# Kernel tuning notes

Measured on AMD Instinct MI355X. Metric: run time of the kernel, lower is better.

Reference implementation:

```python
import jax, jax.numpy as jnp
import numpy as np


def lut_quantize(v, lut):
    """Nearest-neighbor LUT quantization with straight-through estimator.
    lut is sorted ascending; uses searchsorted (no [N, L] blowup)."""
    L = lut.shape[0]
    idx = jnp.clip(jnp.searchsorted(lut, v), 1, L - 1)
    left = jnp.take(lut, idx - 1)
    right = jnp.take(lut, idx)
    q = jnp.where(v - left <= right - v, left, right)
    return v + jax.lax.stop_gradient(q - v)


def mem_conv(x, w, b, lut):
    # memConv2d: weights/bias snapped to LUT levels, then standard 3x3 SAME conv (NCHW/OIHW)
    wq = lut_quantize(w, lut)
    bq = lut_quantize(b, lut)
    y = jax.lax.conv_general_dilated(x, wq, window_strides=(1, 1),
                                     padding=((1, 1), (1, 1)),
                                     dimension_numbers=('NCHW', 'OIHW', 'NCHW'))
    return y + bq[None, :, None, None]


def mem_linear(x, w, b, lut):
    # memLinear: torch-style weight (out, in)
    return x @ lut_quantize(w, lut).T + lut_quantize(b, lut)


def mem_relu(x, lut):
    # memReLu: ReLU followed by LUT quantization of the activation
    return lut_quantize(jnp.maximum(x, 0.0), lut)


def max_pool_2x2(x):
    return jax.lax.reduce_window(x, -jnp.inf, jax.lax.max,
                                 (1, 1, 2, 2), (1, 1, 2, 2), 'VALID')


def _forward(x, lut, w1, b1, w2, b2, w3, b3, w4, b4, w5, b5, w6, b6,
             fw1, fb1, fw2, fb2, fw3, fb3):
    x = mem_relu(mem_conv(x, w1, b1, lut), lut)
    x = mem_relu(mem_conv(x, w2, b2, lut), lut)
    x = max_pool_2x2(x)                      # [B,32,16,16]
    x = mem_relu(mem_conv(x, w3, b3, lut), lut)
    x = mem_relu(mem_conv(x, w4, b4, lut), lut)
    x = max_pool_2x2(x)                      # [B,64,8,8]
    x = mem_relu(mem_conv(x, w5, b5, lut), lut)
    x = mem_relu(mem_conv(x, w6, b6, lut), lut)
    x = max_pool_2x2(x)                      # [B,128,4,4]
    x = x.reshape(-1, 128 * 4 * 4)
    x = mem_relu(mem_linear(x, fw1, fb1, lut), lut)
    x = mem_relu(mem_linear(x, fw2, fb2, lut), lut)
    x = mem_linear(x, fw3, fb3, lut)
    return jax.nn.softmax(x, axis=1)


def setup_inputs() -> dict:
    key = jax.random.key(0)
    ks = jax.random.split(key, 20)
    B = 512
    lut = jnp.linspace(-4.0, 4.0, 129).astype(jnp.float32)

    def conv_w(k, co, ci):
        scale = np.sqrt(2.0 / (ci * 9)).astype(np.float32)
        return jax.random.normal(k, (co, ci, 3, 3), jnp.float32) * scale

    def lin_w(k, co, ci):
        scale = np.sqrt(2.0 / ci).astype(np.float32)
        return jax.random.normal(k, (co, ci), jnp.float32) * scale

    return {
        'x': jax.random.normal(ks[0], (B, 3, 32, 32), jnp.float32),
        'lut': lut,
        'w1': conv_w(ks[1], 32, 3),   'b1': jnp.zeros((32,), jnp.float32),
        'w2': conv_w(ks[2], 32, 32),  'b2': jnp.zeros((32,), jnp.float32),
        'w3': conv_w(ks[3], 64, 32),  'b3': jnp.zeros((64,), jnp.float32),
        'w4': conv_w(ks[4], 64, 64),  'b4': jnp.zeros((64,), jnp.float32),
        'w5': conv_w(ks[5], 128, 64), 'b5': jnp.zeros((128,), jnp.float32),
        'w6': conv_w(ks[6], 128, 128),'b6': jnp.zeros((128,), jnp.float32),
        'fw1': lin_w(ks[7], 512, 2048), 'fb1': jnp.zeros((512,), jnp.float32),
        'fw2': lin_w(ks[8], 128, 512),  'fb2': jnp.zeros((128,), jnp.float32),
        'fw3': lin_w(ks[9], 10, 128),   'fb3': jnp.zeros((10,), jnp.float32),
    }


def reference(x, lut, w1, b1, w2, b2, w3, b3, w4, b4, w5, b5, w6, b6,
              fw1, fb1, fw2, fb2, fw3, fb3):
    return _forward(x, lut, w1, b1, w2, b2, w3, b3, w4, b4, w5, b5, w6, b6,
                    fw1, fb1, fw2, fb2, fw3, fb3)
```

## Files before the change

### kernel.cpp

```cpp
#include <hip/hip_runtime.h>
#include <cstddef>


#define B_SZ 512
typedef unsigned int u32;
typedef __attribute__((ext_vector_type(4))) int i32x4;

__device__ __forceinline__ float lutq(float v) {
    float k = ceilf(v * 16.0f - 0.5f);
    k = fminf(64.0f, fmaxf(-64.0f, k));
    return k * 0.0625f;
}
__device__ __forceinline__ int kq(float x) {
    float kf = ceilf(x * 16.0f - 0.5f);
    kf = fminf(64.0f, fmaxf(-64.0f, kf));
    return (int)kf;
}
__device__ __forceinline__ u32 bmax4u(u32 a, u32 b) {
    u32 r = 0;
    #pragma unroll
    for (int j = 0; j < 4; ++j) {
        u32 x = (a >> (8 * j)) & 255u, y = (b >> (8 * j)) & 255u;
        r |= (x > y ? x : y) << (8 * j);
    }
    return r;
}
__device__ __forceinline__ int requant(int s, int kb16) {
    int vv = s + kb16;
    vv = vv > 0 ? vv : 0;
    int kk = (vv + 7) >> 4;
    return kk > 64 ? 64 : kk;
}

__device__ __forceinline__ void prep_conv_frag(const float* __restrict__ w, char* __restrict__ q,
                                               int i, int CI) {
    int NSTEP = (9 * CI + 63) / 64;
    int e = i & 15, t = i >> 4;
    int ln = t & 63, t2 = t >> 6;
    int s = t2 % NSTEP, co_tile = t2 / NSTEP;
    int k = s * 64 + ((ln >> 4) << 4) + e;
    int tap = k / CI, ci = k % CI;
    int co = co_tile * 16 + (ln & 15);
    int val = 0;
    if (tap < 9) val = kq(w[(co * CI + ci) * 9 + tap]);
    q[i] = (char)val;
}
__device__ __forceinline__ void prep_fc_frag(const float* __restrict__ w, char* __restrict__ q,
                                             int i, int K) {
    int S = K >> 6;
    int e = i & 15, t = i >> 4;
    int ln = t & 63, t2 = t >> 6;
    int s = t2 % S, n_tile = t2 / S;
    int n = n_tile * 16 + (ln & 15);
    int k = s * 64 + ((ln >> 4) << 4) + e;
    q[i] = (char)kq(w[(size_t)n * K + k]);
}

__global__ __launch_bounds__(256) void prep_conv1(
    const float* __restrict__ w2, const float* __restrict__ w3, const float* __restrict__ w4,
    const float* __restrict__ w5, const float* __restrict__ w6,
    const float* __restrict__ fw1, const float* __restrict__ fw2,
    char* q2, char* q3, char* q4, char* q5, char* q6, char* qf1, char* qf2,
    const float* __restrict__ x, const float* __restrict__ w1,
    const float* __restrict__ b1, char* __restrict__ out)
{
    const int tid = threadIdx.x;
    const int bid = blockIdx.x;
    if (bid < 5480) {
        int i = bid * 256 + tid;
        if (i < 10240)                  { prep_conv_frag(w2, q2, i, 32);  }
        else if ((i -= 10240) < 20480)  { prep_conv_frag(w3, q3, i, 32);  }
        else if ((i -= 20480) < 36864)  { prep_conv_frag(w4, q4, i, 64);  }
        else if ((i -= 36864) < 73728)  { prep_conv_frag(w5, q5, i, 64);  }
        else if ((i -= 73728) < 147456) { prep_conv_frag(w6, q6, i, 128); }
        else if ((i -= 147456) < 1048576){ prep_fc_frag(fw1, qf1, i, 2048); }
        else if ((i -= 1048576) < 65536) { prep_fc_frag(fw2, qf2, i, 512);  }
        return;
    }
    __shared__ float s_w[3][9][32];
    __shared__ float s_b[32];
    __shared__ float s_in[3][10][34];
    const int bx  = bid - 5480;
    const int b   = bx >> 2;
    const int r0  = (bx & 3) * 8;
    for (int i = tid; i < 864; i += 256) {
        int o = i % 32, k = (i / 32) % 9, c = i / 288;
        s_w[c][k][o] = lutq(w1[(o * 3 + c) * 9 + k]);
    }
    if (tid < 32) s_b[tid] = lutq(b1[tid]);
    for (int i = tid; i < 3 * 10 * 34; i += 256) {
        int xx = i % 34, yy = (i / 34) % 10, c = i / 340;
        int gy = r0 + yy - 1, gx = xx - 1;
        float v = 0.f;
        if ((unsigned)gy < 32u && (unsigned)gx < 32u)
            v = x[(((size_t)b * 3 + c) * 32 + gy) * 32 + gx];
        s_in[c][yy][xx] = v;
    }
    __syncthreads();
    const int y = tid >> 5, xx = tid & 31;
    float acc[32];
    #pragma unroll
    for (int o = 0; o < 32; ++o) acc[o] = 0.f;
    #pragma unroll
    for (int c = 0; c < 3; ++c) {
        #pragma unroll
        for (int k = 0; k < 9; ++k) {
            float iv = s_in[c][y + k / 3][xx + k % 3];
            #pragma unroll
            for (int o = 0; o < 32; ++o) acc[o] = fmaf(iv, s_w[c][k][o], acc[o]);
        }
    }
    u32 u[8];
    #pragma unroll
    for (int j = 0; j < 8; ++j) {
        u32 p = 0;
        #pragma unroll
        for (int q = 0; q < 4; ++q) {
            float v = fmaxf(acc[4 * j + q] + s_b[4 * j + q], 0.f);
            int kk = (int)ceilf(v * 16.0f - 0.5f);
            kk = kk > 64 ? 64 : kk;
            p |= ((u32)kk & 255u) << (8 * q);
        }
        u[j] = p;
    }
    const int p = (b << 10) + ((r0 + y) << 5) + xx;
    u32* o4 = (u32*)(out + (size_t)p * 32);
    #pragma unroll
    for (int j = 0; j < 8; ++j) o4[j] = u[j];
}

template<int HW, int CI, int CO, int RS, int NIMG, int NT, int POOL = 0>
__global__ __launch_bounds__(256) void conv_mfma(
    const char* __restrict__ in, const char* __restrict__ wq,
    const float* __restrict__ bias, char* __restrict__ out)
{
    constexpr int PH  = HW + 2;
    constexpr int PIX = NIMG * (RS + 2) * PH;
    constexpr int M   = NIMG * RS * HW;
    constexpr int MT  = M / 16;
    constexpr int MW  = MT / 4;
    constexpr int NSTEP = (9 * CI + 63) / 64;
    constexpr int SL  = HW / RS;
    constexpr int NC16 = CI / 16;
    constexpr int NTC = NT * 16;

    __shared__ __align__(128) char s_in[PIX * CI];

    const int tid = threadIdx.x;
    const int g   = blockIdx.x;
    const int b0  = (g / SL) * NIMG;
    const int r0  = (g % SL) * RS;
    const int co0 = blockIdx.y * NTC;

    constexpr int TOTC = PIX * NC16;
    for (int i = tid; i < TOTC; i += 256) {
        int c16 = i % NC16;
        int pp  = i / NC16;
        int xx  = pp % PH;
        int rr  = pp / PH;
        int yy  = rr % (RS + 2);
        int img = rr / (RS + 2);
        int gy = r0 + yy - 1, gx = xx - 1;
        uint4 v = {0u, 0u, 0u, 0u};
        if ((unsigned)gy < (unsigned)HW && (unsigned)gx < (unsigned)HW)
            v = *(const uint4*)(in + ((((size_t)(b0 + img) * HW + gy) * HW + gx) * CI + c16 * 16));
        int off = (pp * CI + c16 * 16) ^ ((pp & 7) << 4);
        *(uint4*)(s_in + off) = v;
    }
    __syncthreads();

    const int wv = tid >> 6, ln = tid & 63;
    const int l15 = ln & 15, lq = ln >> 4;

    int ppad[MW];
    #pragma unroll
    for (int mw = 0; mw < MW; ++mw) {
        int p = (wv * MW + mw) * 16 + l15;
        int img = p / (RS * HW);
        int rem = p % (RS * HW);
        int ly = rem / HW, lx = rem % HW;
        ppad[mw] = (img * (RS + 2) + ly + 1) * PH + lx + 1;
    }

    i32x4 acc[MW][NT] = {};
    const char* wtile = wq + ((size_t)blockIdx.y * NT) * NSTEP * 1024 + (ln << 4);
    auto dp = [](int t) { return (t / 3 - 1) * PH + (t % 3 - 1); };

    #pragma unroll
    for (int s = 0; s < NSTEP; ++s) {
        i32x4 bf[NT];
        #pragma unroll
        for (int nt = 0; nt < NT; ++nt)
            bf[nt] = *(const i32x4*)(wtile + ((nt * NSTEP + s) << 10));
        int dd, ci0;
        if constexpr (CI == 32) {
            int d0 = dp(2 * s);
            int d1 = (2 * s + 1 < 9) ? dp(2 * s + 1) : 0;
            dd  = (lq & 2) ? d1 : d0;
            ci0 = (lq & 1) << 4;
        } else if constexpr (CI == 64) {
            dd  = dp(s);
            ci0 = lq << 4;
        } else {
            dd  = dp(s >> 1);
            ci0 = ((s & 1) << 6) + (lq << 4);
        }
        #pragma unroll
        for (int mw = 0; mw < MW; ++mw) {
            int pix = ppad[mw] + dd;
            int off = (pix * CI + ci0) ^ ((pix & 7) << 4);
            i32x4 af = *(const i32x4*)(s_in + off);
            #pragma unroll
            for (int nt = 0; nt < NT; ++nt)
                acc[mw][nt] = __builtin_amdgcn_mfma_i32_16x16x64_i8(af, bf[nt], acc[mw][nt], 0, 0, 0);
        }
    }

    if constexpr (POOL == 0) {
        #pragma unroll
        for (int nt = 0; nt < NT; ++nt) {
            int kb16 = 16 * kq(bias[co0 + nt * 16 + l15]);
            #pragma unroll
            for (int mw = 0; mw < MW; ++mw)
                #pragma unroll
                for (int r = 0; r < 4; ++r) {
                    int p = (wv * MW + mw) * 16 + lq * 4 + r;
                    int img = p / (RS * HW), rem = p % (RS * HW);
                    int ly = rem / HW, lx = rem % HW;
                    out[(((size_t)(b0 + img) * HW + r0 + ly) * HW + lx) * CO + co0 + nt * 16 + l15] =
                        (char)requant(acc[mw][nt][r], kb16);
                }
        }
    } else {
        __syncthreads();
        char* s_out = s_in;
        #pragma unroll
        for (int nt = 0; nt < NT; ++nt) {
            int kb16 = 16 * kq(bias[co0 + nt * 16 + l15]);
            #pragma unroll
            for (int mw = 0; mw < MW; ++mw)
                #pragma unroll
                for (int r = 0; r < 4; ++r) {
                    int p = (wv * MW + mw) * 16 + lq * 4 + r;
                    s_out[p * NTC + nt * 16 + l15] = (char)requant(acc[mw][nt][r], kb16);
                }
        }
        __syncthreads();
        constexpr int PR = RS / 2, PC = HW / 2, HOW = HW / 2;
        constexpr int OCT = NIMG * PR * PC * (NTC / 16);
        for (int idx = tid; idx < OCT; idx += 256) {
            int c16 = idx % (NTC / 16);
            int pp  = idx / (NTC / 16);
            int xo = pp % PC, yo = (pp / PC) % PR, img = pp / (PC * PR);
            int pb = (img * RS + 2 * yo) * HW + 2 * xo;
            uint4 v0 = *(const uint4*)(s_out + (pb)          * NTC + c16 * 16);
            uint4 v1 = *(const uint4*)(s_out + (pb + 1)      * NTC + c16 * 16);
            uint4 v2 = *(const uint4*)(s_out + (pb + HW)     * NTC + c16 * 16);
            uint4 v3 = *(const uint4*)(s_out + (pb + HW + 1) * NTC + c16 * 16);
            uint4 r;
            r.x = bmax4u(bmax4u(v0.x, v1.x), bmax4u(v2.x, v3.x));
            r.y = bmax4u(bmax4u(v0.y, v1.y), bmax4u(v2.y, v3.y));
            r.z = bmax4u(bmax4u(v0.z, v1.z), bmax4u(v2.z, v3.z));
            r.w = bmax4u(bmax4u(v0.w, v1.w), bmax4u(v2.w, v3.w));
            *(uint4*)(out + ((((size_t)(b0 + img) * HOW + (r0 >> 1) + yo) * HOW + xo) * CO
                             + co0 + c16 * 16)) = r;
        }
    }
}

__global__ __launch_bounds__(256) void conv34(
    const char* __restrict__ in,
    const char* __restrict__ q3, const float* __restrict__ b3,
    const char* __restrict__ q4, const float* __restrict__ b4,
    char* __restrict__ out)
{
    __shared__ __align__(128) char s_in[18 * 18 * 32];
    __shared__ __align__(128) char mid[18 * 18 * 64];
    const int tid = threadIdx.x;
    const int b   = blockIdx.x;
    const int wv = tid >> 6, ln = tid & 63, l15 = ln & 15, lq = ln >> 4;

    for (int i = tid; i < 648; i += 256) {
        int c16 = i & 1;
        int pp  = i >> 1;
        int xx = pp % 18, yy = pp / 18;
        int gy = yy - 1, gx = xx - 1;
        uint4 v = {0u, 0u, 0u, 0u};
        if ((unsigned)gy < 16u && (unsigned)gx < 16u)
            v = *(const uint4*)(in + (((size_t)b * 16 + gy) * 16 + gx) * 32 + c16 * 16);
        int off = (pp * 32 + c16 * 16) ^ ((pp & 7) << 4);
        *(uint4*)(s_in + off) = v;
    }
    for (int i = tid; i < 5184; i += 256) ((u32*)mid)[i] = 0u;
    __syncthreads();

    int ppad[4];
    #pragma unroll
    for (int mw = 0; mw < 4; ++mw) {
        int p = (wv * 4 + mw) * 16 + l15;
        ppad[mw] = ((p >> 4) + 1) * 18 + (p & 15) + 1;
    }
    auto dp18 = [](int t) { return (t / 3 - 1) * 18 + (t % 3 - 1); };

    i32x4 acc3[4][4] = {};
    #pragma unroll
    for (int s = 0; s < 5; ++s) {
        i32x4 bf[4];
        #pragma unroll
        for (int nt = 0; nt < 4; ++nt)
            bf[nt] = *(const i32x4*)(q3 + ((nt * 5 + s) << 10) + (ln << 4));
        int d0 = dp18(2 * s);
        int d1 = (2 * s + 1 < 9) ? dp18(2 * s + 1) : 0;
        int dd = (lq & 2) ? d1 : d0;
        int ci0 = (lq & 1) << 4;
        #pragma unroll
        for (int mw = 0; mw < 4; ++mw) {
            int pix = ppad[mw] + dd;
            int off = (pix * 32 + ci0) ^ ((pix & 7) << 4);
            i32x4 af = *(const i32x4*)(s_in + off);
            #pragma unroll
            for (int nt = 0; nt < 4; ++nt)
                acc3[mw][nt] = __builtin_amdgcn_mfma_i32_16x16x64_i8(af, bf[nt], acc3[mw][nt], 0, 0, 0);
        }
    }
    #pragma unroll
    for (int nt = 0; nt < 4; ++nt) {
        int kb16 = 16 * kq(b3[nt * 16 + l15]);
        #pragma unroll
        for (int mw = 0; mw < 4; ++mw)
            #pragma unroll
            for (int r = 0; r < 4; ++r) {
                int p = (wv * 4 + mw) * 16 + lq * 4 + r;
                int pix = ((p >> 4) + 1) * 18 + (p & 15) + 1;
                mid[(pix * 64 + nt * 16 + l15) ^ ((pix & 7) << 4)] =
                    (char)requant(acc3[mw][nt][r], kb16);
            }
    }
    __syncthreads();

    i32x4 acc4[4][4] = {};
    #pragma unroll
    for (int s = 0; s < 9; ++s) {
        i32x4 bf[4];
        #pragma unroll
        for (int nt = 0; nt < 4; ++nt)
            bf[nt] = *(const i32x4*)(q4 + ((nt * 9 + s) << 10) + (ln << 4));
        int dd = dp18(s);
        int ci0 = lq << 4;
        #pragma unroll
        for (int mw = 0; mw < 4; ++mw) {
            int pix = ppad[mw] + dd;
            int off = (pix * 64 + ci0) ^ ((pix & 7) << 4);
            i32x4 af = *(const i32x4*)(mid + off);
            #pragma unroll
            for (int nt = 0; nt < 4; ++nt)
                acc4[mw][nt] = __builtin_amdgcn_mfma_i32_16x16x64_i8(af, bf[nt], acc4[mw][nt], 0, 0, 0);
        }
    }
    __syncthreads();
    char* s_out = mid;
    #pragma unroll
    for (int nt = 0; nt < 4; ++nt) {
        int kb16 = 16 * kq(b4[nt * 16 + l15]);
        #pragma unroll
        for (int mw = 0; mw < 4; ++mw)
            #pragma unroll
            for (int r = 0; r < 4; ++r) {
                int p = (wv * 4 + mw) * 16 + lq * 4 + r;
                s_out[p * 64 + nt * 16 + l15] = (char)requant(acc4[mw][nt][r], kb16);
            }
    }
    __syncthreads();
    {
        int c16 = tid & 3;
        int pp  = tid >> 2;
        int xo = pp & 7, yo = pp >> 3;
        int pb = (2 * yo) * 16 + 2 * xo;
        uint4 v0 = *(const uint4*)(s_out + (pb)      * 64 + c16 * 16);
        uint4 v1 = *(const uint4*)(s_out + (pb + 1)  * 64 + c16 * 16);
        uint4 v2 = *(const uint4*)(s_out + (pb + 16) * 64 + c16 * 16);
        uint4 v3 = *(const uint4*)(s_out + (pb + 17) * 64 + c16 * 16);
        uint4 r;
        r.x = bmax4u(bmax4u(v0.x, v1.x), bmax4u(v2.x, v3.x));
        r.y = bmax4u(bmax4u(v0.y, v1.y), bmax4u(v2.y, v3.y));
        r.z = bmax4u(bmax4u(v0.z, v1.z), bmax4u(v2.z, v3.z));
        r.w = bmax4u(bmax4u(v0.w, v1.w), bmax4u(v2.w, v3.w));
        *(uint4*)(out + (((size_t)b * 8 + yo) * 8 + xo) * 64 + c16 * 16) = r;
    }
}

__global__ __launch_bounds__(256) void conv56(
    const char* __restrict__ in,
    const char* __restrict__ q5, const float* __restrict__ b5,
    const char* __restrict__ q6, const float* __restrict__ b6,
    char* __restrict__ fc1a)
{
    __shared__ __align__(128) char sA[8192];
    __shared__ __align__(128) char sB[12800];
    const int tid = threadIdx.x;
    const int b   = blockIdx.x;
    const int wv = tid >> 6, ln = tid & 63, l15 = ln & 15, lq = ln >> 4;

    for (int i = tid; i < 400; i += 256) {
        int c16 = i & 3;
        int pp  = i >> 2;
        int xx = pp % 10, yy = pp / 10;
        int gy = yy - 1, gx = xx - 1;
        uint4 v = {0u, 0u, 0u, 0u};
        if ((unsigned)gy < 8u && (unsigned)gx < 8u)
            v = *(const uint4*)(in + (((size_t)b * 8 + gy) * 8 + gx) * 64 + c16 * 16);
        int off = (pp * 64 + c16 * 16) ^ ((pp & 7) << 4);
        *(uint4*)(sA + off) = v;
    }
    for (int i = tid; i < 3200; i += 256) ((u32*)sB)[i] = 0u;
    __syncthreads();

    const int p0 = wv * 16 + l15;
    const int ppad = ((p0 >> 3) + 1) * 10 + (p0 & 7) + 1;
    auto dp10 = [](int t) { return (t / 3 - 1) * 10 + (t % 3 - 1); };

    i32x4 acc5[8] = {};
    #pragma unroll
    for (int s = 0; s < 9; ++s) {
        i32x4 bf[8];
        #pragma unroll
        for (int nt = 0; nt < 8; ++nt)
            bf[nt] = *(const i32x4*)(q5 + ((nt * 9 + s) << 10) + (ln << 4));
        int dd = dp10(s);
        int ci0 = lq << 4;
        int pix = ppad + dd;
        int off = (pix * 64 + ci0) ^ ((pix & 7) << 4);
        i32x4 af = *(const i32x4*)(sA + off);
        #pragma unroll
        for (int nt = 0; nt < 8; ++nt)
            acc5[nt] = __builtin_amdgcn_mfma_i32_16x16x64_i8(af, bf[nt], acc5[nt], 0, 0, 0);
    }
    #pragma unroll
    for (int nt = 0; nt < 8; ++nt) {
        int kb16 = 16 * kq(b5[nt * 16 + l15]);
        #pragma unroll
        for (int r = 0; r < 4; ++r) {
            int p = wv * 16 + lq * 4 + r;
            int pix = ((p >> 3) + 1) * 10 + (p & 7) + 1;
            sB[(pix * 128 + nt * 16 + l15) ^ ((pix & 7) << 4)] =
                (char)requant(acc5[nt][r], kb16);
        }
    }
    __syncthreads();

    i32x4 acc6[8] = {};
    #pragma unroll
    for (int s = 0; s < 18; ++s) {
        i32x4 bf[8];
        #pragma unroll
        for (int nt = 0; nt < 8; ++nt)
            bf[nt] = *(const i32x4*)(q6 + ((nt * 18 + s) << 10) + (ln << 4));
        int dd = dp10(s >> 1);
        int ci0 = ((s & 1) << 6) + (lq << 4);
        int pix = ppad + dd;
        int off = (pix * 128 + ci0) ^ ((pix & 7) << 4);
        i32x4 af = *(const i32x4*)(sB + off);
        #pragma unroll
        for (int nt = 0; nt < 8; ++nt)
            acc6[nt] = __builtin_amdgcn_mfma_i32_16x16x64_i8(af, bf[nt], acc6[nt], 0, 0, 0);
    }
    __syncthreads();
    char* s_out = sA;
    #pragma unroll
    for (int nt = 0; nt < 8; ++nt) {
        int kb16 = 16 * kq(b6[nt * 16 + l15]);
        #pragma unroll
        for (int r = 0; r < 4; ++r) {
            int p = wv * 16 + lq * 4 + r;
            s_out[p * 128 + nt * 16 + l15] = (char)requant(acc6[nt][r], kb16);
        }
    }
    __syncthreads();
    if (tid < 128) {
        int c16 = tid & 7;
        int pp  = tid >> 3;
        int xo = pp & 3, yo = pp >> 2;
        int pb = (2 * yo) * 8 + 2 * xo;
        uint4 v0 = *(const uint4*)(s_out + (pb)     * 128 + c16 * 16);
        uint4 v1 = *(const uint4*)(s_out + (pb + 1) * 128 + c16 * 16);
        uint4 v2 = *(const uint4*)(s_out + (pb + 8) * 128 + c16 * 16);
        uint4 v3 = *(const uint4*)(s_out + (pb + 9) * 128 + c16 * 16);
        uint4 r;
        r.x = bmax4u(bmax4u(v0.x, v1.x), bmax4u(v2.x, v3.x));
        r.y = bmax4u(bmax4u(v0.y, v1.y), bmax4u(v2.y, v3.y));
        r.z = bmax4u(bmax4u(v0.z, v1.z), bmax4u(v2.z, v3.z));
        r.w = bmax4u(bmax4u(v0.w, v1.w), bmax4u(v2.w, v3.w));
        const char* rv = (const char*)&r;
        int m = b;
        #pragma unroll
        for (int j = 0; j < 16; ++j) {
            int c = c16 * 16 + j;
            int k = c * 16 + yo * 4 + xo;
            int off = (((m >> 4) * 32 + (k >> 6)) << 10)
                    + ((((k >> 4) & 3) * 16 + (m & 15)) << 4) + (k & 15);
            fc1a[off] = rv[j];
        }
    }
}

template<int N, int K, int SK>
__global__ __launch_bounds__(256) void fc1_splitk(
    const char* __restrict__ xa, const char* __restrict__ wq, int* __restrict__ part)
{
    constexpr int KCH = K / SK;
    constexpr int KS = K / 64;
    const int tid = threadIdx.x, wv = tid >> 6, ln = tid & 63;
    const int l15 = ln & 15, lq = ln >> 4;
    const int m0 = blockIdx.x * 128, n0 = blockIdx.y * 128;
    const int kb = blockIdx.z * KCH;
    const int mq = (wv >> 1) * 4, nq = (wv & 1) * 4;
    i32x4 acc[4][4] = {};
    const char* xr[4];
    const char* wt[4];
    #pragma unroll
    for (int t = 0; t < 4; ++t) {
        xr[t] = xa + (size_t)((m0 >> 4) + mq + t) * KS * 1024 + (ln << 4);
        wt[t] = wq + (size_t)((n0 >> 4) + nq + t) * KS * 1024 + (ln << 4);
    }
    for (int k0 = 0; k0 < KCH; k0 += 64) {
        const int s = (kb + k0) >> 6;
        i32x4 a[4], b[4];
        #pragma unroll
        for (int t = 0; t < 4; ++t) {
            a[t] = *(const i32x4*)(xr[t] + (s << 10));
            b[t] = *(const i32x4*)(wt[t] + (s << 10));
        }
        #pragma unroll
        for (int i = 0; i < 4; ++i)
            #pragma unroll
            for (int j = 0; j < 4; ++j)
                acc[i][j] = __builtin_amdgcn_mfma_i32_16x16x64_i8(a[i], b[j], acc[i][j], 0, 0, 0);
    }
    int* pb = part + (size_t)blockIdx.z * (B_SZ * N);
    #pragma unroll
    for (int j = 0; j < 4; ++j) {
        int n = n0 + (nq + j) * 16 + l15;
        #pragma unroll
        for (int i = 0; i < 4; ++i)
            #pragma unroll
            for (int r = 0; r < 4; ++r) {
                int m = m0 + (mq + i) * 16 + lq * 4 + r;
                pb[(size_t)m * N + n] = acc[i][j][r];
            }
    }
}

template<int N, int SK>
__global__ __launch_bounds__(256) void fc_reduce(
    const int* __restrict__ part, const float* __restrict__ bias, char* __restrict__ out)
{
    int i = blockIdx.x * 256 + threadIdx.x;
    if (i >= B_SZ * N) return;
    int s = 0;
    #pragma unroll
    for (int k = 0; k < SK; ++k) s += part[(size_t)k * (B_SZ * N) + i];
    out[i] = (char)requant(s, 16 * kq(bias[i % N]));
}

__global__ __launch_bounds__(256) void fc_tail(
    const char* __restrict__ x, const char* __restrict__ qf2,
    const float* __restrict__ fb2, const float* __restrict__ fw3,
    const float* __restrict__ fb3, float* __restrict__ out)
{
    __shared__ __align__(16) char sx[16 * 512];
    __shared__ __align__(16) char sy[16 * 128];
    __shared__ __align__(16) char sw3[10 * 128];
    __shared__ float sb3[10];
    __shared__ int sp[16][16][10];

    const int tid = threadIdx.x;
    const int m0 = blockIdx.x * 16;

    for (int idx = tid; idx < 512; idx += 256) {
        int r = idx >> 5, c16 = idx & 31;
        uint4 v = *(const uint4*)(x + (size_t)(m0 + r) * 512 + c16 * 16);
        *(uint4*)(sx + ((r * 512 + c16 * 16) ^ ((r & 7) << 4))) = v;
    }
    for (int i = tid; i < 1280; i += 256) sw3[i] = (char)kq(fw3[i]);
    if (tid < 10) sb3[tid] = lutq(fb3[tid]);
    __syncthreads();

    const int wv = tid >> 6, ln = tid & 63, l15 = ln & 15, lq = ln >> 4;
    const int ntg = wv * 2;
    i32x4 acc[2] = {};
    #pragma unroll
    for (int s = 0; s < 8; ++s) {
        int row = l15;
        i32x4 a = *(const i32x4*)(sx + ((row * 512 + s * 64 + lq * 16) ^ ((row & 7) << 4)));
        #pragma unroll
        for (int nt = 0; nt < 2; ++nt) {
            i32x4 b = *(const i32x4*)(qf2 + (((ntg + nt) * 8 + s) << 10) + (ln << 4));
            acc[nt] = __builtin_amdgcn_mfma_i32_16x16x64_i8(a, b, acc[nt], 0, 0, 0);
        }
    }
    #pragma unroll
    for (int nt = 0; nt < 2; ++nt) {
        int n = (ntg + nt) * 16 + l15;
        int kb16 = 16 * kq(fb2[n]);
        #pragma unroll
        for (int r = 0; r < 4; ++r) {
            int row = lq * 4 + r;
            sy[(row * 128 + n) ^ ((row & 7) << 4)] = (char)requant(acc[nt][r], kb16);
        }
    }
    __syncthreads();

    {
        int r = tid >> 4, g = tid & 15;
        uint2 yv = *(const uint2*)(sy + ((r * 128 + g * 8) ^ ((r & 7) << 4)));
        const char* yb = (const char*)&yv;
        #pragma unroll
        for (int o = 0; o < 10; ++o) {
            uint2 wv2 = *(const uint2*)(sw3 + o * 128 + g * 8);
            const char* wb = (const char*)&wv2;
            int S = 0;
            #pragma unroll
            for (int e = 0; e < 8; ++e) S += (int)yb[e] * (int)wb[e];
            sp[r][g][o] = S;
        }
    }
    __syncthreads();

    if (tid < 16) {
        int r = tid;
        float d[10];
        #pragma unroll
        for (int o = 0; o < 10; ++o) {
            int S = 0;
            #pragma unroll
            for (int g = 0; g < 16; ++g) S += sp[r][g][o];
            d[o] = (float)S * 0.00390625f + sb3[o];
        }
        float m = d[0];
        #pragma unroll
        for (int o = 1; o < 10; ++o) m = fmaxf(m, d[o]);
        float e[10];
        float sum = 0.f;
        #pragma unroll
        for (int o = 0; o < 10; ++o) { e[o] = expf(d[o] - m); sum += e[o]; }
        #pragma unroll
        for (int o = 0; o < 10; ++o) out[(size_t)(m0 + r) * 10 + o] = e[o] / sum;
    }
}

extern "C" void kernel_launch(void* const* d_in, const int* in_sizes, int n_in,
                              void* d_out, int out_size, void* d_ws, size_t ws_size,
                              hipStream_t stream)
{
    const float* x   = (const float*)d_in[0];
    const float* w1  = (const float*)d_in[2];
    const float* b1  = (const float*)d_in[3];
    const float* w2  = (const float*)d_in[4];
    const float* b2  = (const float*)d_in[5];
    const float* w3  = (const float*)d_in[6];
    const float* b3  = (const float*)d_in[7];
    const float* w4  = (const float*)d_in[8];
    const float* b4  = (const float*)d_in[9];
    const float* w5  = (const float*)d_in[10];
    const float* b5  = (const float*)d_in[11];
    const float* w6  = (const float*)d_in[12];
    const float* b6  = (const float*)d_in[13];
    const float* fw1 = (const float*)d_in[14];
    const float* fb1 = (const float*)d_in[15];
    const float* fw2 = (const float*)d_in[16];
    const float* fb2 = (const float*)d_in[17];
    const float* fw3 = (const float*)d_in[18];
    const float* fb3 = (const float*)d_in[19];
    float* out = (float*)d_out;

    char* bufA = (char*)d_ws;
    char* bufB = bufA + (16u << 20);
    char* q2  = bufB + (16u << 20);
    char* q3  = q2 + 10240;
    char* q4  = q3 + 20480;
    char* q5  = q4 + 36864;
    char* q6  = q5 + 73728;
    char* qf1 = q6 + 147456;
    char* qf2 = qf1 + 1048576;
    int*  part = (int*)(qf2 + 65536);
    char* fc1out = (char*)part + (16u << 20);
    char* fc1a   = fc1out + 262144;

    dim3 blk(256);

    prep_conv1<<<dim3(7528), blk, 0, stream>>>(
        w2, w3, w4, w5, w6, fw1, fw2, q2, q3, q4, q5, q6, qf1, qf2,
        x, w1, b1, bufA);
    conv_mfma<32, 32, 32, 8, 1, 2, 1><<<dim3(2048, 1), blk, 0, stream>>>(bufA, q2, b2, bufB);
    conv34<<<dim3(512), blk, 0, stream>>>(bufB, q3, b3, q4, b4, bufA);
    conv56<<<dim3(512), blk, 0, stream>>>(bufA, q5, b5, q6, b6, fc1a);
    fc1_splitk<512, 2048, 16><<<dim3(4, 4, 16), blk, 0, stream>>>(fc1a, qf1, part);
    fc_reduce<512, 16><<<dim3(1024), blk, 0, stream>>>(part, fb1, fc1out);
    fc_tail<<<dim3(32), blk, 0, stream>>>(fc1out, qf2, fb2, fw3, fb3, out);
}
```

Measured before the change: 97.43 us.

## Fuse all six conv layers into one per-image megakernel and fold FC1 reduce into tail

Replaces the separate conv1, conv2, conv34 and conv56 kernels with a single kernel that keeps each image's activations in shared memory through all conv and pooling stages. This removes the global-memory round trips of intermediate int8 activations and several kernel launches. The split-K reduction for FC1 is also folded into the tail kernel. The trade-off is only 512 blocks with about 64KB of shared memory each, which limits occupancy. The FC1 reduction is now done by just 32 blocks that read 16 partial sums per element.

```diff
diff --git a/kernel.cpp b/kernel.cpp
--- a/kernel.cpp
+++ b/kernel.cpp
@@ -56,441 +56,341 @@
     q[i] = (char)kq(w[(size_t)n * K + k]);
 }
 
-__global__ __launch_bounds__(256) void prep_conv1(
+__global__ __launch_bounds__(256) void prep_weights(
     const float* __restrict__ w2, const float* __restrict__ w3, const float* __restrict__ w4,
     const float* __restrict__ w5, const float* __restrict__ w6,
     const float* __restrict__ fw1, const float* __restrict__ fw2,
-    char* q2, char* q3, char* q4, char* q5, char* q6, char* qf1, char* qf2,
-    const float* __restrict__ x, const float* __restrict__ w1,
-    const float* __restrict__ b1, char* __restrict__ out)
+    char* q2, char* q3, char* q4, char* q5, char* q6, char* qf1, char* qf2)
 {
+    int i = blockIdx.x * 256 + threadIdx.x;
+    if (i < 10240)                  { prep_conv_frag(w2, q2, i, 32);  }
+    else if ((i -= 10240) < 20480)  { prep_conv_frag(w3, q3, i, 32);  }
+    else if ((i -= 20480) < 36864)  { prep_conv_frag(w4, q4, i, 64);  }
+    else if ((i -= 36864) < 73728)  { prep_conv_frag(w5, q5, i, 64);  }
+    else if ((i -= 73728) < 147456) { prep_conv_frag(w6, q6, i, 128); }
+    else if ((i -= 147456) < 1048576){ prep_fc_frag(fw1, qf1, i, 2048); }
+    else if ((i -= 1048576) < 65536) { prep_fc_frag(fw2, qf2, i, 512);  }
+}
+
+__global__ __launch_bounds__(256, 2) void megaconv(
+    const float* __restrict__ x, const float* __restrict__ w1, const float* __restrict__ b1,
+    const char* __restrict__ q2, const float* __restrict__ b2,
+    const char* __restrict__ q3, const float* __restrict__ b3,
+    const char* __restrict__ q4, const float* __restrict__ b4,
+    const char* __restrict__ q5, const float* __restrict__ b5,
+    const char* __restrict__ q6, const float* __restrict__ b6,
+    char* __restrict__ fc1a)
+{
+    __shared__ __align__(128) char smem[64816];
+    float* X  = (float*)smem;
+    float* SW = (float*)(smem + 13872);
+    float* SB = (float*)(smem + 17328);
+    char*  C1 = smem + 17456;
+    char*  C2 = smem;
+    char*  C3 = smem + 54448;
+    char*  C4 = smem;
+    char*  C5 = smem + 20736;
+    char*  C6 = smem + 54448;
+    char*  C7 = smem;
+    char*  C8 = smem + 12800;
+
     const int tid = threadIdx.x;
-    const int bid = blockIdx.x;
-    if (bid < 5480) {
-        int i = bid * 256 + tid;
-        if (i < 10240)                  { prep_conv_frag(w2, q2, i, 32);  }
-        else if ((i -= 10240) < 20480)  { prep_conv_frag(w3, q3, i, 32);  }
-        else if ((i -= 20480) < 36864)  { prep_conv_frag(w4, q4, i, 64);  }
-        else if ((i -= 36864) < 73728)  { prep_conv_frag(w5, q5, i, 64);  }
-        else if ((i -= 73728) < 147456) { prep_conv_frag(w6, q6, i, 128); }
-        else if ((i -= 147456) < 1048576){ prep_fc_frag(fw1, qf1, i, 2048); }
-        else if ((i -= 1048576) < 65536) { prep_fc_frag(fw2, qf2, i, 512);  }
-        return;
-    }
-    __shared__ float s_w[3][9][32];
-    __shared__ float s_b[32];
-    __shared__ float s_in[3][10][34];
-    const int bx  = bid - 5480;
-    const int b   = bx >> 2;
-    const int r0  = (bx & 3) * 8;
-    for (int i = tid; i < 864; i += 256) {
-        int o = i % 32, k = (i / 32) % 9, c = i / 288;
-        s_w[c][k][o] = lutq(w1[(o * 3 + c) * 9 + k]);
-    }
-    if (tid < 32) s_b[tid] = lutq(b1[tid]);
-    for (int i = tid; i < 3 * 10 * 34; i += 256) {
-        int xx = i % 34, yy = (i / 34) % 10, c = i / 340;
-        int gy = r0 + yy - 1, gx = xx - 1;
+    const int b   = blockIdx.x;
+    const int wv = tid >> 6, ln = tid & 63, l15 = ln & 15, lq = ln >> 4;
+
+    auto dp34 = [](int t) { return (t / 3 - 1) * 34 + (t % 3 - 1); };
+    auto dp18 = [](int t) { return (t / 3 - 1) * 18 + (t % 3 - 1); };
+    auto dp10 = [](int t) { return (t / 3 - 1) * 10 + (t % 3 - 1); };
+
+    for (int i = tid; i < 3468; i += 256) {
+        int xx = i % 34, t = i / 34, yy = t % 34, c = t / 34;
+        int gy = yy - 1, gx = xx - 1;
         float v = 0.f;
         if ((unsigned)gy < 32u && (unsigned)gx < 32u)
             v = x[(((size_t)b * 3 + c) * 32 + gy) * 32 + gx];
-        s_in[c][yy][xx] = v;
-    }
-    __syncthreads();
-    const int y = tid >> 5, xx = tid & 31;
-    float acc[32];
-    #pragma unroll
-    for (int o = 0; o < 32; ++o) acc[o] = 0.f;
-    #pragma unroll
-    for (int c = 0; c < 3; ++c) {
-        #pragma unroll
-        for (int k = 0; k < 9; ++k) {
-            float iv = s_in[c][y + k / 3][xx + k % 3];
-            #pragma unroll
-            for (int o = 0; o < 32; ++o) acc[o] = fmaf(iv, s_w[c][k][o], acc[o]);
-        }
-    }
-    u32 u[8];
-    #pragma unroll
-    for (int j = 0; j < 8; ++j) {
-        u32 p = 0;
-        #pragma unroll
-        for (int q = 0; q < 4; ++q) {
-            float v = fmaxf(acc[4 * j + q] + s_b[4 * j + q], 0.f);
-            int kk = (int)ceilf(v * 16.0f - 0.5f);
-            kk = kk > 64 ? 64 : kk;
-            p |= ((u32)kk & 255u) << (8 * q);
-        }
-        u[j] = p;
-    }
-    const int p = (b << 10) + ((r0 + y) << 5) + xx;
-    u32* o4 = (u32*)(out + (size_t)p * 32);
-    #pragma unroll
-    for (int j = 0; j < 8; ++j) o4[j] = u[j];
-}
-
-template<int HW, int CI, int CO, int RS, int NIMG, int NT, int POOL = 0>
-__global__ __launch_bounds__(256) void conv_mfma(
-    const char* __restrict__ in, const char* __restrict__ wq,
-    const float* __restrict__ bias, char* __restrict__ out)
-{
-    constexpr int PH  = HW + 2;
-    constexpr int PIX = NIMG * (RS + 2) * PH;
-    constexpr int M   = NIMG * RS * HW;
-    constexpr int MT  = M / 16;
-    constexpr int MW  = MT / 4;
-    constexpr int NSTEP = (9 * CI + 63) / 64;
-    constexpr int SL  = HW / RS;
-    constexpr int NC16 = CI / 16;
-    constexpr int NTC = NT * 16;
-
-    __shared__ __align__(128) char s_in[PIX * CI];
-
-    const int tid = threadIdx.x;
-    const int g   = blockIdx.x;
-    const int b0  = (g / SL) * NIMG;
-    const int r0  = (g % SL) * RS;
-    const int co0 = blockIdx.y * NTC;
-
-    constexpr int TOTC = PIX * NC16;
-    for (int i = tid; i < TOTC; i += 256) {
-        int c16 = i % NC16;
-        int pp  = i / NC16;
-        int xx  = pp % PH;
-        int rr  = pp / PH;
-        int yy  = rr % (RS + 2);
-        int img = rr / (RS + 2);
-        int gy = r0 + yy - 1, gx = xx - 1;
-        uint4 v = {0u, 0u, 0u, 0u};
-        if ((unsigned)gy < (unsigned)HW && (unsigned)gx < (unsigned)HW)
-            v = *(const uint4*)(in + ((((size_t)(b0 + img) * HW + gy) * HW + gx) * CI + c16 * 16));
-        int off = (pp * CI + c16 * 16) ^ ((pp & 7) << 4);
-        *(uint4*)(s_in + off) = v;
-    }
-    __syncthreads();
-
-    const int wv = tid >> 6, ln = tid & 63;
-    const int l15 = ln & 15, lq = ln >> 4;
-
-    int ppad[MW];
-    #pragma unroll
-    for (int mw = 0; mw < MW; ++mw) {
-        int p = (wv * MW + mw) * 16 + l15;
-        int img = p / (RS * HW);
-        int rem = p % (RS * HW);
-        int ly = rem / HW, lx = rem % HW;
-        ppad[mw] = (img * (RS + 2) + ly + 1) * PH + lx + 1;
-    }
-
-    i32x4 acc[MW][NT] = {};
-    const char* wtile = wq + ((size_t)blockIdx.y * NT) * NSTEP * 1024 + (ln << 4);
-    auto dp = [](int t) { return (t / 3 - 1) * PH + (t % 3 - 1); };
-
-    #pragma unroll
-    for (int s = 0; s < NSTEP; ++s) {
-        i32x4 bf[NT];
-        #pragma unroll
-        for (int nt = 0; nt < NT; ++nt)
-            bf[nt] = *(const i32x4*)(wtile + ((nt * NSTEP + s) << 10));
-        int dd, ci0;
-        if constexpr (CI == 32) {
-            int d0 = dp(2 * s);
-            int d1 = (2 * s + 1 < 9) ? dp(2 * s + 1) : 0;
-            dd  = (lq & 2) ? d1 : d0;
-            ci0 = (lq & 1) << 4;
-        } else if constexpr (CI == 64) {
-            dd  = dp(s);
-            ci0 = lq << 4;
-        } else {
-            dd  = dp(s >> 1);
-            ci0 = ((s & 1) << 6) + (lq << 4);
-        }
-        #pragma unroll
-        for (int mw = 0; mw < MW; ++mw) {
-            int pix = ppad[mw] + dd;
-            int off = (pix * CI + ci0) ^ ((pix & 7) << 4);
-            i32x4 af = *(const i32x4*)(s_in + off);
-            #pragma unroll
-            for (int nt = 0; nt < NT; ++nt)
-                acc[mw][nt] = __builtin_amdgcn_mfma_i32_16x16x64_i8(af, bf[nt], acc[mw][nt], 0, 0, 0);
-        }
-    }
-
-    if constexpr (POOL == 0) {
-        #pragma unroll
-        for (int nt = 0; nt < NT; ++nt) {
-            int kb16 = 16 * kq(bias[co0 + nt * 16 + l15]);
-            #pragma unroll
-            for (int mw = 0; mw < MW; ++mw)
+        X[i] = v;
+    }
+    for (int i = tid; i < 864; i += 256) {
+        int o = i % 32, k = (i / 32) % 9, c = i / 288;
+        SW[(c * 9 + k) * 32 + o] = lutq(w1[(o * 3 + c) * 9 + k]);
+    }
+    if (tid < 32) SB[tid] = lutq(b1[tid]);
+    for (int i = tid; i < 9248; i += 256) ((u32*)C1)[i] = 0u;
+    for (int i = tid; i < 2592; i += 256) ((u32*)C3)[i] = 0u;
+    __syncthreads();
+
+    for (int qq = 0; qq < 4; ++qq) {
+        int p = qq * 256 + tid;
+        int y = p >> 5, xc = p & 31;
+        float acc[32];
+        #pragma unroll
+        for (int o = 0; o < 32; ++o) acc[o] = 0.f;
+        #pragma unroll
+        for (int c = 0; c < 3; ++c)
+            #pragma unroll
+            for (int k = 0; k < 9; ++k) {
+                float iv = X[(c * 34 + y + k / 3) * 34 + xc + k % 3];
+                #pragma unroll
+                for (int o = 0; o < 32; ++o) acc[o] = fmaf(iv, SW[(c * 9 + k) * 32 + o], acc[o]);
+            }
+        int pix = (y + 1) * 34 + xc + 1;
+        #pragma unroll
+        for (int j = 0; j < 2; ++j) {
+            uint4 pk;
+            u32* pw = (u32*)&pk;
+            #pragma unroll
+            for (int h = 0; h < 4; ++h) {
+                u32 w = 0;
+                #pragma unroll
+                for (int e = 0; e < 4; ++e) {
+                    float v = fmaxf(acc[j * 16 + h * 4 + e] + SB[j * 16 + h * 4 + e], 0.f);
+                    int kk = (int)ceilf(v * 16.0f - 0.5f);
+                    kk = kk > 64 ? 64 : kk;
+                    w |= ((u32)kk & 255u) << (8 * e);
+                }
+                pw[h] = w;
+            }
+            *(uint4*)(C1 + ((pix * 32 + j * 16) ^ ((pix & 7) << 4))) = pk;
+        }
+    }
+    __syncthreads();
+
+    for (int r0 = 0; r0 < 32; r0 += 8) {
+        int ppad2[4];
+        #pragma unroll
+        for (int mw = 0; mw < 4; ++mw) {
+            int p = (wv * 4 + mw) * 16 + l15;
+            ppad2[mw] = (r0 + (p >> 5) + 1) * 34 + (p & 31) + 1;
+        }
+        i32x4 acc[4][2] = {};
+        #pragma unroll
+        for (int s = 0; s < 5; ++s) {
+            i32x4 bf[2];
+            #pragma unroll
+            for (int nt = 0; nt < 2; ++nt)
+                bf[nt] = *(const i32x4*)(q2 + (((nt * 5 + s) << 10) + (ln << 4)));
+            int d0 = dp34(2 * s);
+            int d1 = (2 * s + 1 < 9) ? dp34(2 * s + 1) : 0;
+            int dd = (lq & 2) ? d1 : d0;
+            int ci0 = (lq & 1) << 4;
+            #pragma unroll
+            for (int mw = 0; mw < 4; ++mw) {
+                int pix = ppad2[mw] + dd;
+                i32x4 af = *(const i32x4*)(C1 + ((pix * 32 + ci0) ^ ((pix & 7) << 4)));
+                #pragma unroll
+                for (int nt = 0; nt < 2; ++nt)
+                    acc[mw][nt] = __builtin_amdgcn_mfma_i32_16x16x64_i8(af, bf[nt], acc[mw][nt], 0, 0, 0);
+            }
+        }
+        #pragma unroll
+        for (int nt = 0; nt < 2; ++nt) {
+            int kb16 = 16 * kq(b2[nt * 16 + l15]);
+            #pragma unroll
+            for (int mw = 0; mw < 4; ++mw)
                 #pragma unroll
                 for (int r = 0; r < 4; ++r) {
-                    int p = (wv * MW + mw) * 16 + lq * 4 + r;
-                    int img = p / (RS * HW), rem = p % (RS * HW);
-                    int ly = rem / HW, lx = rem % HW;
-                    out[(((size_t)(b0 + img) * HW + r0 + ly) * HW + lx) * CO + co0 + nt * 16 + l15] =
-                        (char)requant(acc[mw][nt][r], kb16);
+                    int p = (wv * 4 + mw) * 16 + lq * 4 + r;
+                    C2[p * 32 + nt * 16 + l15] = (char)requant(acc[mw][nt][r], kb16);
                 }
         }
-    } else {
         __syncthreads();
-        char* s_out = s_in;
-        #pragma unroll
-        for (int nt = 0; nt < NT; ++nt) {
-            int kb16 = 16 * kq(bias[co0 + nt * 16 + l15]);
-            #pragma unroll
-            for (int mw = 0; mw < MW; ++mw)
-                #pragma unroll
-                for (int r = 0; r < 4; ++r) {
-                    int p = (wv * MW + mw) * 16 + lq * 4 + r;
-                    s_out[p * NTC + nt * 16 + l15] = (char)requant(acc[mw][nt][r], kb16);
-                }
+        if (tid < 128) {
+            int c16 = tid & 1;
+            int pp  = tid >> 1;
+            int xo = pp & 15, yo = pp >> 4;
+            int pb = (2 * yo) * 32 + 2 * xo;
+            uint4 v0 = *(const uint4*)(C2 + (pb)      * 32 + c16 * 16);
+            uint4 v1 = *(const uint4*)(C2 + (pb + 1)  * 32 + c16 * 16);
+            uint4 v2 = *(const uint4*)(C2 + (pb + 32) * 32 + c16 * 16);
+            uint4 v3 = *(const uint4*)(C2 + (pb + 33) * 32 + c16 * 16);
+            uint4 rr;
+            rr.x = bmax4u(bmax4u(v0.x, v1.x), bmax4u(v2.x, v3.x));
+            rr.y = bmax4u(bmax4u(v0.y, v1.y), bmax4u(v2.y, v3.y));
+            rr.z = bmax4u(bmax4u(v0.z, v1.z), bmax4u(v2.z, v3.z));
+            rr.w = bmax4u(bmax4u(v0.w, v1.w), bmax4u(v2.w, v3.w));
+            int py = (r0 >> 1) + yo;
+            int c3pix = (py + 1) * 18 + xo + 1;
+            *(uint4*)(C3 + ((c3pix * 32 + c16 * 16) ^ ((c3pix & 7) << 4))) = rr;
         }
         __syncthreads();
-        constexpr int PR = RS / 2, PC = HW / 2, HOW = HW / 2;
-        constexpr int OCT = NIMG * PR * PC * (NTC / 16);
-        for (int idx = tid; idx < OCT; idx += 256) {
-            int c16 = idx % (NTC / 16);
-            int pp  = idx / (NTC / 16);
-            int xo = pp % PC, yo = (pp / PC) % PR, img = pp / (PC * PR);
-            int pb = (img * RS + 2 * yo) * HW + 2 * xo;
-            uint4 v0 = *(const uint4*)(s_out + (pb)          * NTC + c16 * 16);
-            uint4 v1 = *(const uint4*)(s_out + (pb + 1)      * NTC + c16 * 16);
-            uint4 v2 = *(const uint4*)(s_out + (pb + HW)     * NTC + c16 * 16);
-            uint4 v3 = *(const uint4*)(s_out + (pb + HW + 1) * NTC + c16 * 16);
-            uint4 r;
-            r.x = bmax4u(bmax4u(v0.x, v1.x), bmax4u(v2.x, v3.x));
-            r.y = bmax4u(bmax4u(v0.y, v1.y), bmax4u(v2.y, v3.y));
-            r.z = bmax4u(bmax4u(v0.z, v1.z), bmax4u(v2.z, v3.z));
-            r.w = bmax4u(bmax4u(v0.w, v1.w), bmax4u(v2.w, v3.w));
-            *(uint4*)(out + ((((size_t)(b0 + img) * HOW + (r0 >> 1) + yo) * HOW + xo) * CO
-                             + co0 + c16 * 16)) = r;
-        }
-    }
-}
-
-__global__ __launch_bounds__(256) void conv34(
-    const char* __restrict__ in,
-    const char* __restrict__ q3, const float* __restrict__ b3,
-    const char* __restrict__ q4, const float* __restrict__ b4,
-    char* __restrict__ out)
-{
-    __shared__ __align__(128) char s_in[18 * 18 * 32];
-    __shared__ __align__(128) char mid[18 * 18 * 64];
-    const int tid = threadIdx.x;
-    const int b   = blockIdx.x;
-    const int wv = tid >> 6, ln = tid & 63, l15 = ln & 15, lq = ln >> 4;
-
-    for (int i = tid; i < 648; i += 256) {
-        int c16 = i & 1;
-        int pp  = i >> 1;
-        int xx = pp % 18, yy = pp / 18;
-        int gy = yy - 1, gx = xx - 1;
-        uint4 v = {0u, 0u, 0u, 0u};
-        if ((unsigned)gy < 16u && (unsigned)gx < 16u)
-            v = *(const uint4*)(in + (((size_t)b * 16 + gy) * 16 + gx) * 32 + c16 * 16);
-        int off = (pp * 32 + c16 * 16) ^ ((pp & 7) << 4);
-        *(uint4*)(s_in + off) = v;
-    }
-    for (int i = tid; i < 5184; i += 256) ((u32*)mid)[i] = 0u;
-    __syncthreads();
-
-    int ppad[4];
+    }
+
+    for (int i = tid; i < 5184; i += 256) ((u32*)C4)[i] = 0u;
+    __syncthreads();
+
+    int ppad16[4];
     #pragma unroll
     for (int mw = 0; mw < 4; ++mw) {
         int p = (wv * 4 + mw) * 16 + l15;
-        ppad[mw] = ((p >> 4) + 1) * 18 + (p & 15) + 1;
-    }
-    auto dp18 = [](int t) { return (t / 3 - 1) * 18 + (t % 3 - 1); };
-
-    i32x4 acc3[4][4] = {};
-    #pragma unroll
-    for (int s = 0; s < 5; ++s) {
-        i32x4 bf[4];
-        #pragma unroll
-        for (int nt = 0; nt < 4; ++nt)
-            bf[nt] = *(const i32x4*)(q3 + ((nt * 5 + s) << 10) + (ln << 4));
-        int d0 = dp18(2 * s);
-        int d1 = (2 * s + 1 < 9) ? dp18(2 * s + 1) : 0;
-        int dd = (lq & 2) ? d1 : d0;
-        int ci0 = (lq & 1) << 4;
-        #pragma unroll
-        for (int mw = 0; mw < 4; ++mw) {
-            int pix = ppad[mw] + dd;
-            int off = (pix * 32 + ci0) ^ ((pix & 7) << 4);
-            i32x4 af = *(const i32x4*)(s_in + off);
+        ppad16[mw] = ((p >> 4) + 1) * 18 + (p & 15) + 1;
+    }
+
+    {
+        i32x4 acc3[4][4] = {};
+        #pragma unroll
+        for (int s = 0; s < 5; ++s) {
+            i32x4 bf[4];
             #pragma unroll
             for (int nt = 0; nt < 4; ++nt)
-                acc3[mw][nt] = __builtin_amdgcn_mfma_i32_16x16x64_i8(af, bf[nt], acc3[mw][nt], 0, 0, 0);
-        }
-    }
-    #pragma unroll
-    for (int nt = 0; nt < 4; ++nt) {
-        int kb16 = 16 * kq(b3[nt * 16 + l15]);
-        #pragma unroll
-        for (int mw = 0; mw < 4; ++mw)
-            #pragma unroll
-            for (int r = 0; r < 4; ++r) {
-                int p = (wv * 4 + mw) * 16 + lq * 4 + r;
-                int pix = ((p >> 4) + 1) * 18 + (p & 15) + 1;
-                mid[(pix * 64 + nt * 16 + l15) ^ ((pix & 7) << 4)] =
-                    (char)requant(acc3[mw][nt][r], kb16);
-            }
-    }
-    __syncthreads();
-
-    i32x4 acc4[4][4] = {};
-    #pragma unroll
-    for (int s = 0; s < 9; ++s) {
-        i32x4 bf[4];
-        #pragma unroll
-        for (int nt = 0; nt < 4; ++nt)
-            bf[nt] = *(const i32x4*)(q4 + ((nt * 9 + s) << 10) + (ln << 4));
-        int dd = dp18(s);
-        int ci0 = lq << 4;
-        #pragma unroll
-        for (int mw = 0; mw < 4; ++mw) {
-            int pix = ppad[mw] + dd;
-            int off = (pix * 64 + ci0) ^ ((pix & 7) << 4);
-            i32x4 af = *(const i32x4*)(mid + off);
+                bf[nt] = *(const i32x4*)(q3 + (((nt * 5 + s) << 10) + (ln << 4)));
+            int d0 = dp18(2 * s);
+            int d1 = (2 * s + 1 < 9) ? dp18(2 * s + 1) : 0;
+            int dd = (lq & 2) ? d1 : d0;
+            int ci0 = (lq & 1) << 4;
+            #pragma unroll
+            for (int mw = 0; mw < 4; ++mw) {
+                int pix = ppad16[mw] + dd;
+                i32x4 af = *(const i32x4*)(C3 + ((pix * 32 + ci0) ^ ((pix & 7) << 4)));
+                #pragma unroll
+                for (int nt = 0; nt < 4; ++nt)
+                    acc3[mw][nt] = __builtin_amdgcn_mfma_i32_16x16x64_i8(af, bf[nt], acc3[mw][nt], 0, 0, 0);
+            }
+        }
+        #pragma unroll
+        for (int nt = 0; nt < 4; ++nt) {
+            int kb16 = 16 * kq(b3[nt * 16 + l15]);
+            #pragma unroll
+            for (int mw = 0; mw < 4; ++mw)
+                #pragma unroll
+                for (int r = 0; r < 4; ++r) {
+                    int p = (wv * 4 + mw) * 16 + lq * 4 + r;
+                    int pix = ((p >> 4) + 1) * 18 + (p & 15) + 1;
+                    C4[(pix * 64 + nt * 16 + l15) ^ ((pix & 7) << 4)] =
+                        (char)requant(acc3[mw][nt][r], kb16);
+                }
+        }
+    }
+    __syncthreads();
+
+    {
+        i32x4 acc4[4][4] = {};
+        #pragma unroll
+        for (int s = 0; s < 9; ++s) {
+            i32x4 bf[4];
             #pragma unroll
             for (int nt = 0; nt < 4; ++nt)
-                acc4[mw][nt] = __builtin_amdgcn_mfma_i32_16x16x64_i8(af, bf[nt], acc4[mw][nt], 0, 0, 0);
-        }
-    }
-    __syncthreads();
-    char* s_out = mid;
-    #pragma unroll
-    for (int nt = 0; nt < 4; ++nt) {
-        int kb16 = 16 * kq(b4[nt * 16 + l15]);
-        #pragma unroll
-        for (int mw = 0; mw < 4; ++mw)
-            #pragma unroll
-            for (int r = 0; r < 4; ++r) {
-                int p = (wv * 4 + mw) * 16 + lq * 4 + r;
-                s_out[p * 64 + nt * 16 + l15] = (char)requant(acc4[mw][nt][r], kb16);
-            }
-    }
-    __syncthreads();
+                bf[nt] = *(const i32x4*)(q4 + (((nt * 9 + s) << 10) + (ln << 4)));
+            int dd = dp18(s);
+            int ci0 = lq << 4;
+            #pragma unroll
+            for (int mw = 0; mw < 4; ++mw) {
+                int pix = ppad16[mw] + dd;
+                i32x4 af = *(const i32x4*)(C4 + ((pix * 64 + ci0) ^ ((pix & 7) << 4)));
+                #pragma unroll
+                for (int nt = 0; nt < 4; ++nt)
+                    acc4[mw][nt] = __builtin_amdgcn_mfma_i32_16x16x64_i8(af, bf[nt], acc4[mw][nt], 0, 0, 0);
+            }
+        }
+        #pragma unroll
+        for (int nt = 0; nt < 4; ++nt) {
+            int kb16 = 16 * kq(b4[nt * 16 + l15]);
+            #pragma unroll
+            for (int mw = 0; mw < 4; ++mw)
+                #pragma unroll
+                for (int r = 0; r < 4; ++r) {
+                    int p = (wv * 4 + mw) * 16 + lq * 4 + r;
+                    C5[p * 64 + nt * 16 + l15] = (char)requant(acc4[mw][nt][r], kb16);
+                }
+        }
+    }
+    for (int i = tid; i < 1600; i += 256) ((u32*)C6)[i] = 0u;
+    __syncthreads();
+
     {
         int c16 = tid & 3;
         int pp  = tid >> 2;
         int xo = pp & 7, yo = pp >> 3;
         int pb = (2 * yo) * 16 + 2 * xo;
-        uint4 v0 = *(const uint4*)(s_out + (pb)      * 64 + c16 * 16);
-        uint4 v1 = *(const uint4*)(s_out + (pb + 1)  * 64 + c16 * 16);
-        uint4 v2 = *(const uint4*)(s_out + (pb + 16) * 64 + c16 * 16);
-        uint4 v3 = *(const uint4*)(s_out + (pb + 17) * 64 + c16 * 16);
-        uint4 r;
-        r.x = bmax4u(bmax4u(v0.x, v1.x), bmax4u(v2.x, v3.x));
-        r.y = bmax4u(bmax4u(v0.y, v1.y), bmax4u(v2.y, v3.y));
-        r.z = bmax4u(bmax4u(v0.z, v1.z), bmax4u(v2.z, v3.z));
-        r.w = bmax4u(bmax4u(v0.w, v1.w), bmax4u(v2.w, v3.w));
-        *(uint4*)(out + (((size_t)b * 8 + yo) * 8 + xo) * 64 + c16 * 16) = r;
-    }
-}
-
-__global__ __launch_bounds__(256) void conv56(
-    const char* __restrict__ in,
-    const char* __restrict__ q5, const float* __restrict__ b5,
-    const char* __restrict__ q6, const float* __restrict__ b6,
-    char* __restrict__ fc1a)
-{
-    __shared__ __align__(128) char sA[8192];
-    __shared__ __align__(128) char sB[12800];
-    const int tid = threadIdx.x;
-    const int b   = blockIdx.x;
-    const int wv = tid >> 6, ln = tid & 63, l15 = ln & 15, lq = ln >> 4;
-
-    for (int i = tid; i < 400; i += 256) {
-        int c16 = i & 3;
-        int pp  = i >> 2;
-        int xx = pp % 10, yy = pp / 10;
-        int gy = yy - 1, gx = xx - 1;
-        uint4 v = {0u, 0u, 0u, 0u};
-        if ((unsigned)gy < 8u && (unsigned)gx < 8u)
-            v = *(const uint4*)(in + (((size_t)b * 8 + gy) * 8 + gx) * 64 + c16 * 16);
-        int off = (pp * 64 + c16 * 16) ^ ((pp & 7) << 4);
-        *(uint4*)(sA + off) = v;
-    }
-    for (int i = tid; i < 3200; i += 256) ((u32*)sB)[i] = 0u;
+        uint4 v0 = *(const uint4*)(C5 + (pb)      * 64 + c16 * 16);
+        uint4 v1 = *(const uint4*)(C5 + (pb + 1)  * 64 + c16 * 16);
+        uint4 v2 = *(const uint4*)(C5 + (pb + 16) * 64 + c16 * 16);
+        uint4 v3 = *(const uint4*)(C5 + (pb + 17) * 64 + c16 * 16);
+        uint4 rr;
+        rr.x = bmax4u(bmax4u(v0.x, v1.x), bmax4u(v2.x, v3.x));
+        rr.y = bmax4u(bmax4u(v0.y, v1.y), bmax4u(v2.y, v3.y));
+        rr.z = bmax4u(bmax4u(v0.z, v1.z), bmax4u(v2.z, v3.z));
+        rr.w = bmax4u(bmax4u(v0.w, v1.w), bmax4u(v2.w, v3.w));
+        int c6pix = (yo + 1) * 10 + xo + 1;
+        *(uint4*)(C6 + ((c6pix * 64 + c16 * 16) ^ ((c6pix & 7) << 4))) = rr;
+    }
+    for (int i = tid; i < 3200; i += 256) ((u32*)C7)[i] = 0u;
     __syncthreads();
 
     const int p0 = wv * 16 + l15;
-    const int ppad = ((p0 >> 3) + 1) * 10 + (p0 & 7) + 1;
-    auto dp10 = [](int t) { return (t / 3 - 1) * 10 + (t % 3 - 1); };
-
-    i32x4 acc5[8] = {};
-    #pragma unroll
-    for (int s = 0; s < 9; ++s) {
-        i32x4 bf[8];
-        #pragma unroll
-        for (int nt = 0; nt < 8; ++nt)
-            bf[nt] = *(const i32x4*)(q5 + ((nt * 9 + s) << 10) + (ln << 4));
-        int dd = dp10(s);
-        int ci0 = lq << 4;
-        int pix = ppad + dd;
-        int off = (pix * 64 + ci0) ^ ((pix & 7) << 4);
-        i32x4 af = *(const i32x4*)(sA + off);
-        #pragma unroll
-        for (int nt = 0; nt < 8; ++nt)
-            acc5[nt] = __builtin_amdgcn_mfma_i32_16x16x64_i8(af, bf[nt], acc5[nt], 0, 0, 0);
-    }
-    #pragma unroll
-    for (int nt = 0; nt < 8; ++nt) {
-        int kb16 = 16 * kq(b5[nt * 16 + l15]);
-        #pragma unroll
-        for (int r = 0; r < 4; ++r) {
-            int p = wv * 16 + lq * 4 + r;
-            int pix = ((p >> 3) + 1) * 10 + (p & 7) + 1;
-            sB[(pix * 128 + nt * 16 + l15) ^ ((pix & 7) << 4)] =
-                (char)requant(acc5[nt][r], kb16);
-        }
-    }
-    __syncthreads();
-
-    i32x4 acc6[8] = {};
-    #pragma unroll
-    for (int s = 0; s < 18; ++s) {
-        i32x4 bf[8];
-        #pragma unroll
-        for (int nt = 0; nt < 8; ++nt)
-            bf[nt] = *(const i32x4*)(q6 + ((nt * 18 + s) << 10) + (ln << 4));
-        int dd = dp10(s >> 1);
-        int ci0 = ((s & 1) << 6) + (lq << 4);
-        int pix = ppad + dd;
-        int off = (pix * 128 + ci0) ^ ((pix & 7) << 4);
-        i32x4 af = *(const i32x4*)(sB + off);
-        #pragma unroll
-        for (int nt = 0; nt < 8; ++nt)
-            acc6[nt] = __builtin_amdgcn_mfma_i32_16x16x64_i8(af, bf[nt], acc6[nt], 0, 0, 0);
-    }
-    __syncthreads();
-    char* s_out = sA;
-    #pragma unroll
-    for (int nt = 0; nt < 8; ++nt) {
-        int kb16 = 16 * kq(b6[nt * 16 + l15]);
-        #pragma unroll
-        for (int r = 0; r < 4; ++r) {
-            int p = wv * 16 + lq * 4 + r;
-            s_out[p * 128 + nt * 16 + l15] = (char)requant(acc6[nt][r], kb16);
-        }
-    }
-    __syncthreads();
+    const int ppad10 = ((p0 >> 3) + 1) * 10 + (p0 & 7) + 1;
+    {
+        i32x4 acc5[8] = {};
+        #pragma unroll
+        for (int s = 0; s < 9; ++s) {
+            i32x4 bf[8];
+            #pragma unroll
+            for (int nt = 0; nt < 8; ++nt)
+                bf[nt] = *(const i32x4*)(q5 + (((nt * 9 + s) << 10) + (ln << 4)));
+            int dd = dp10(s);
+            int ci0 = lq << 4;
+            int pix = ppad10 + dd;
+            i32x4 af = *(const i32x4*)(C6 + ((pix * 64 + ci0) ^ ((pix & 7) << 4)));
+            #pragma unroll
+            for (int nt = 0; nt < 8; ++nt)
+                acc5[nt] = __builtin_amdgcn_mfma_i32_16x16x64_i8(af, bf[nt], acc5[nt], 0, 0, 0);
+        }
+        #pragma unroll
+        for (int nt = 0; nt < 8; ++nt) {
+            int kb16 = 16 * kq(b5[nt * 16 + l15]);
+            #pragma unroll
+            for (int r = 0; r < 4; ++r) {
+                int p = wv * 16 + lq * 4 + r;
+                int pix = ((p >> 3) + 1) * 10 + (p & 7) + 1;
+                C7[(pix * 128 + nt * 16 + l15) ^ ((pix & 7) << 4)] =
+                    (char)requant(acc5[nt][r], kb16);
+            }
+        }
+    }
+    __syncthreads();
+
+    {
+        i32x4 acc6[8] = {};
+        #pragma unroll
+        for (int s = 0; s < 18; ++s) {
+            i32x4 bf[8];
+            #pragma unroll
+            for (int nt = 0; nt < 8; ++nt)
+                bf[nt] = *(const i32x4*)(q6 + (((nt * 18 + s) << 10) + (ln << 4)));
+            int dd = dp10(s >> 1);
+            int ci0 = ((s & 1) << 6) + (lq << 4);
+            int pix = ppad10 + dd;
+            i32x4 af = *(const i32x4*)(C7 + ((pix * 128 + ci0) ^ ((pix & 7) << 4)));
+            #pragma unroll
+            for (int nt = 0; nt < 8; ++nt)
+                acc6[nt] = __builtin_amdgcn_mfma_i32_16x16x64_i8(af, bf[nt], acc6[nt], 0, 0, 0);
+        }
+        #pragma unroll
+        for (int nt = 0; nt < 8; ++nt) {
+            int kb16 = 16 * kq(b6[nt * 16 + l15]);
+            #pragma unroll
+            for (int r = 0; r < 4; ++r) {
+                int p = wv * 16 + lq * 4 + r;
+                C8[p * 128 + nt * 16 + l15] = (char)requant(acc6[nt][r], kb16);
+            }
+        }
+    }
+    __syncthreads();
+
     if (tid < 128) {
         int c16 = tid & 7;
         int pp  = tid >> 3;
         int xo = pp & 3, yo = pp >> 2;
         int pb = (2 * yo) * 8 + 2 * xo;
-        uint4 v0 = *(const uint4*)(s_out + (pb)     * 128 + c16 * 16);
-        uint4 v1 = *(const uint4*)(s_out + (pb + 1) * 128 + c16 * 16);
-        uint4 v2 = *(const uint4*)(s_out + (pb + 8) * 128 + c16 * 16);
-        uint4 v3 = *(const uint4*)(s_out + (pb + 9) * 128 + c16 * 16);
-        uint4 r;
-        r.x = bmax4u(bmax4u(v0.x, v1.x), bmax4u(v2.x, v3.x));
-        r.y = bmax4u(bmax4u(v0.y, v1.y), bmax4u(v2.y, v3.y));
-        r.z = bmax4u(bmax4u(v0.z, v1.z), bmax4u(v2.z, v3.z));
-        r.w = bmax4u(bmax4u(v0.w, v1.w), bmax4u(v2.w, v3.w));
-        const char* rv = (const char*)&r;
+        uint4 v0 = *(const uint4*)(C8 + (pb)     * 128 + c16 * 16);
+        uint4 v1 = *(const uint4*)(C8 + (pb + 1) * 128 + c16 * 16);
+        uint4 v2 = *(const uint4*)(C8 + (pb + 8) * 128 + c16 * 16);
+        uint4 v3 = *(const uint4*)(C8 + (pb + 9) * 128 + c16 * 16);
+        uint4 rr;
+        rr.x = bmax4u(bmax4u(v0.x, v1.x), bmax4u(v2.x, v3.x));
+        rr.y = bmax4u(bmax4u(v0.y, v1.y), bmax4u(v2.y, v3.y));
+        rr.z = bmax4u(bmax4u(v0.z, v1.z), bmax4u(v2.z, v3.z));
+        rr.w = bmax4u(bmax4u(v0.w, v1.w), bmax4u(v2.w, v3.w));
+        const char* rv = (const char*)&rr;
         int m = b;
         #pragma unroll
         for (int j = 0; j < 16; ++j) {
@@ -550,22 +450,11 @@
     }
 }
 
-template<int N, int SK>
-__global__ __launch_bounds__(256) void fc_reduce(
-    const int* __restrict__ part, const float* __restrict__ bias, char* __restrict__ out)
-{
-    int i = blockIdx.x * 256 + threadIdx.x;
-    if (i >= B_SZ * N) return;
-    int s = 0;
-    #pragma unroll
-    for (int k = 0; k < SK; ++k) s += part[(size_t)k * (B_SZ * N) + i];
-    out[i] = (char)requant(s, 16 * kq(bias[i % N]));
-}
-
 __global__ __launch_bounds__(256) void fc_tail(
-    const char* __restrict__ x, const char* __restrict__ qf2,
-    const float* __restrict__ fb2, const float* __restrict__ fw3,
-    const float* __restrict__ fb3, float* __restrict__ out)
+    const int* __restrict__ part, const float* __restrict__ fb1,
+    const char* __restrict__ qf2, const float* __restrict__ fb2,
+    const float* __restrict__ fw3, const float* __restrict__ fb3,
+    float* __restrict__ out)
 {
     __shared__ __align__(16) char sx[16 * 512];
     __shared__ __align__(16) char sy[16 * 128];
@@ -576,10 +465,13 @@
     const int tid = threadIdx.x;
     const int m0 = blockIdx.x * 16;
 
-    for (int idx = tid; idx < 512; idx += 256) {
-        int r = idx >> 5, c16 = idx & 31;
-        uint4 v = *(const uint4*)(x + (size_t)(m0 + r) * 512 + c16 * 16);
-        *(uint4*)(sx + ((r * 512 + c16 * 16) ^ ((r & 7) << 4))) = v;
+    for (int idx = tid; idx < 8192; idx += 256) {
+        int r = idx >> 9, c = idx & 511;
+        int s = 0;
+        #pragma unroll
+        for (int k = 0; k < 16; ++k)
+            s += part[(size_t)k * (B_SZ * 512) + (size_t)(m0 + r) * 512 + c];
+        sx[(r * 512 + c) ^ ((r & 7) << 4)] = (char)requant(s, 16 * kq(fb1[c]));
     }
     for (int i = tid; i < 1280; i += 256) sw3[i] = (char)kq(fw3[i]);
     if (tid < 10) sb3[tid] = lutq(fb3[tid]);
@@ -673,9 +565,7 @@
     const float* fb3 = (const float*)d_in[19];
     float* out = (float*)d_out;
 
-    char* bufA = (char*)d_ws;
-    char* bufB = bufA + (16u << 20);
-    char* q2  = bufB + (16u << 20);
+    char* q2  = (char*)d_ws;
     char* q3  = q2 + 10240;
     char* q4  = q3 + 20480;
     char* q5  = q4 + 36864;
@@ -683,18 +573,14 @@
     char* qf1 = q6 + 147456;
     char* qf2 = qf1 + 1048576;
     int*  part = (int*)(qf2 + 65536);
-    char* fc1out = (char*)part + (16u << 20);
-    char* fc1a   = fc1out + 262144;
+    char* fc1a = (char*)part + (16u << 20);
 
     dim3 blk(256);
 
-    prep_conv1<<<dim3(7528), blk, 0, stream>>>(
-        w2, w3, w4, w5, w6, fw1, fw2, q2, q3, q4, q5, q6, qf1, qf2,
-        x, w1, b1, bufA);
-    conv_mfma<32, 32, 32, 8, 1, 2, 1><<<dim3(2048, 1), blk, 0, stream>>>(bufA, q2, b2, bufB);
-    conv34<<<dim3(512), blk, 0, stream>>>(bufB, q3, b3, q4, b4, bufA);
-    conv56<<<dim3(512), blk, 0, stream>>>(bufA, q5, b5, q6, b6, fc1a);
+    prep_weights<<<dim3(5480), blk, 0, stream>>>(
+        w2, w3, w4, w5, w6, fw1, fw2, q2, q3, q4, q5, q6, qf1, qf2);
+    megaconv<<<dim3(512), blk, 0, stream>>>(
+        x, w1, b1, q2, b2, q3, b3, q4, b4, q5, b5, q6, b6, fc1a);
     fc1_splitk<512, 2048, 16><<<dim3(4, 4, 16), blk, 0, stream>>>(fc1a, qf1, part);
-    fc_reduce<512, 16><<<dim3(1024), blk, 0, stream>>>(part, fb1, fc1out);
-    fc_tail<<<dim3(32), blk, 0, stream>>>(fc1out, qf2, fb2, fw3, fb3, out);
-}
+    fc_tail<<<dim3(32), blk, 0, stream>>>(part, fb1, qf2, fb2, fw3, fb3, out);
+}
```

Measured after the change: 194.8 us. 99.9% more time.
